# Kernel tuning notes

Hardware: AMD Instinct MI355X
Metric: run time of the kernel (lower is better)

## Reference

```python
import jax, jax.numpy as jnp
import numpy as np
import math

B, T, C = 4, 2048, 2048
HQ, HKV = 16, 4
HD = C // HQ          # 128
REP = HQ // HKV       # 4
EPS = 1e-6


def _rope_tables(seq_len, dim):
    inv_freq = 1.0 / (10000.0 ** (np.arange(0, dim, 2, dtype=np.float32) / dim))
    t = np.arange(seq_len, dtype=np.float32)
    freqs = np.einsum('i,j->ij', t, inv_freq)  # [T, dim/2]
    return jnp.asarray(np.cos(freqs)), jnp.asarray(np.sin(freqs))


def setup_inputs() -> dict:
    key = jax.random.key(0)
    ks = jax.random.split(key, 10)
    s = 0.02
    cos, sin = _rope_tables(T, HD)
    return {
        'x': jax.random.normal(ks[0], (B, T, C), jnp.float32),
        'Wq': jax.random.normal(ks[1], (C, C), jnp.float32) * s,
        'bq': jnp.zeros((C,), jnp.float32),
        'Wk': jax.random.normal(ks[2], (HD * HKV, C), jnp.float32) * s,
        'bk': jnp.zeros((HD * HKV,), jnp.float32),
        'Wv': jax.random.normal(ks[3], (HD * HKV, C), jnp.float32) * s,
        'bv': jnp.zeros((HD * HKV,), jnp.float32),
        'qn_w': jnp.ones((HD,), jnp.float32),
        'kn_w': jnp.ones((HD,), jnp.float32),
        'Wg': jax.random.normal(ks[4], (HD, HD), jnp.float32) * s,
        'bg': jnp.zeros((HD,), jnp.float32),
        'Wo': jax.random.normal(ks[5], (C, C), jnp.float32) * s,
        'bo': jnp.zeros((C,), jnp.float32),
        'cos': cos,
        'sin': sin,
    }


def _apply_rope(x, cos, sin):
    # x: [B,T,H,HD]; cos/sin: [T,HD/2]
    c = cos[None, :, None, :]
    s = sin[None, :, None, :]
    x1, x2 = x[..., ::2], x[..., 1::2]
    return jnp.concatenate([x1 * c - x2 * s, x1 * s + x2 * c], axis=-1)


def _rmsnorm(x, w):
    norm = jnp.mean(x * x, axis=-1, keepdims=True)
    return w * (x * jax.lax.rsqrt(norm + EPS))


def reference(x, Wq, bq, Wk, bk, Wv, bv, qn_w, kn_w, Wg, bg, Wo, bo, cos, sin):
    Bsz, Tlen, _ = x.shape
    q = (x @ Wq.T + bq).reshape(Bsz, Tlen, HQ, HD)
    k = (x @ Wk.T + bk).reshape(Bsz, Tlen, HKV, HD)
    v = (x @ Wv.T + bv).reshape(Bsz, Tlen, HKV, HD)

    q = _rmsnorm(_apply_rope(q, cos, sin), qn_w)
    k = _rmsnorm(_apply_rope(k, cos, sin), kn_w)

    # GQA without materializing repeated K/V: group q heads [B,T,HKV,REP,HD]
    # (repeat_interleave on kv-head dim matches this grouping exactly)
    q5 = q.reshape(Bsz, Tlen, HKV, REP, HD)
    scores = jnp.einsum('btkrd,bskd->bkrts', q5, k) / math.sqrt(HD)

    causal = jnp.tril(jnp.ones((Tlen, Tlen), bool))
    scores = jnp.where(causal, scores, -jnp.inf)
    probs = jax.nn.softmax(scores, axis=-1)

    out = jnp.einsum('bkrts,bskd->btkrd', probs, v).reshape(Bsz, Tlen, HQ, HD)
    gate = jax.nn.sigmoid(out @ Wg.T + bg)
    out = (out * gate).reshape(Bsz, Tlen, C)
    return out @ Wo.T + bo
```

## Files before the change

kernel.cpp:

```cpp
#include <hip/hip_runtime.h>
#include <hip/hip_bf16.h>
#include <math.h>

typedef __attribute__((ext_vector_type(8))) __bf16 bf16x8;
typedef __attribute__((ext_vector_type(4))) float f32x4;

__device__ __forceinline__ void stage16(const void* g, void* l) {
#if __has_builtin(__builtin_amdgcn_global_load_lds)
  __builtin_amdgcn_global_load_lds(
      (const __attribute__((address_space(1))) void*)g,
      (__attribute__((address_space(3))) void*)l, 16, 0, 0);
#else
  *(int4*)l = *(const int4*)g;
#endif
}

__device__ __forceinline__ float sigmoidf_(float x) {
  return 1.0f / (1.0f + __expf(-x));
}

__global__ __launch_bounds__(256) void f2b_kernel(const float* __restrict__ s,
                                                  __bf16* __restrict__ d, int n) {
  int i = (blockIdx.x * blockDim.x + threadIdx.x) * 4;
  if (i >= n) return;
  float4 v = *(const float4*)(s + i);
  union { __bf16 h[4]; int2 p; } u;
  u.h[0] = (__bf16)v.x; u.h[1] = (__bf16)v.y;
  u.h[2] = (__bf16)v.z; u.h[3] = (__bf16)v.w;
  *(int2*)(d + i) = u.p;
}

template <typename OutT>
__global__ __launch_bounds__(512, 1) void gemm256(const __bf16* __restrict__ A,
                                                  const __bf16* __restrict__ Bm,
                                                  const float* __restrict__ bias,
                                                  OutT* __restrict__ C,
                                                  int M, int N, int K, int gx) {
  __shared__ __align__(16) __bf16 Sm[2][2][2][128 * 64];
  const int tid = threadIdx.x, lane = tid & 63, wid = tid >> 6;
  const int wm = wid >> 2, wn = wid & 3;
  const int r = lane & 15, g4 = lane >> 4;
  const int nwg = gridDim.x, qx = nwg >> 3;
  const int wg = (blockIdx.x & 7) * qx + (blockIdx.x >> 3);
  const int m0 = (wg / gx) * 256, n0 = (wg % gx) * 256;

  f32x4 acc[8][4] = {};
  const int NT = K >> 6;

#define STAGE_HALF(buf, which, half, kt)                                          \
  {                                                                               \
    const __bf16* sp_ = (which) ? Bm : A;                                         \
    const int base_ = ((which) ? n0 : m0) + (half) * 128;                         \
    const int k0_ = (kt) << 6;                                                    \
    __bf16* dp_ = &Sm[buf][which][half][0];                                       \
    _Pragma("unroll") for (int i_ = 0; i_ < 2; ++i_) {                            \
      int c_ = i_ * 512 + tid;                                                    \
      int row_ = c_ >> 3, slot_ = c_ & 7;                                         \
      stage16(sp_ + (size_t)(base_ + row_) * K + k0_ + ((slot_ ^ (row_ & 7)) << 3), \
              dp_ + c_ * 8);                                                      \
    }                                                                             \
  }
#define LDSW(base, row, kk) \
  (*(const bf16x8*)&(base)[(row) * 64 + ((((kk) * 4 + g4) ^ ((row) & 7)) << 3)])

  STAGE_HALF(0, 0, 0, 0) STAGE_HALF(0, 0, 1, 0) STAGE_HALF(0, 1, 0, 0) STAGE_HALF(0, 1, 1, 0)

  const int brow = (wn & 1) * 64;
  bf16x8 af[4][2], bfr[2][2];

  for (int kt = 0; kt < NT; ++kt) {
    const int cur = kt & 1, nxt = cur ^ 1;
    const bool more = (kt + 1) < NT;
    const __bf16* Ah = &Sm[cur][0][wm][0];
    const __bf16* Bh = &Sm[cur][1][wn >> 1][0];

    if (more) STAGE_HALF(nxt, 0, 0, kt + 1)
    if (more) { asm volatile("s_waitcnt vmcnt(2)" ::: "memory"); }
    else      { asm volatile("s_waitcnt vmcnt(0)" ::: "memory"); }
    __builtin_amdgcn_s_barrier();
    asm volatile("" ::: "memory");
#pragma unroll
    for (int m = 0; m < 4; ++m)
#pragma unroll
      for (int kk = 0; kk < 2; ++kk) af[m][kk] = LDSW(Ah, m * 16 + r, kk);
#pragma unroll
    for (int n = 0; n < 2; ++n)
#pragma unroll
      for (int kk = 0; kk < 2; ++kk) bfr[n][kk] = LDSW(Bh, brow + n * 16 + r, kk);
    asm volatile("s_waitcnt lgkmcnt(0)" ::: "memory");
    __builtin_amdgcn_sched_barrier(0);
    __builtin_amdgcn_s_setprio(1);
#pragma unroll
    for (int m = 0; m < 4; ++m)
#pragma unroll
      for (int n = 0; n < 2; ++n)
#pragma unroll
        for (int kk = 0; kk < 2; ++kk)
          acc[m][n] = __builtin_amdgcn_mfma_f32_16x16x32_bf16(af[m][kk], bfr[n][kk],
                                                              acc[m][n], 0, 0, 0);
    __builtin_amdgcn_s_setprio(0);
    __builtin_amdgcn_s_barrier();

#pragma unroll
    for (int n = 0; n < 2; ++n)
#pragma unroll
      for (int kk = 0; kk < 2; ++kk) bfr[n][kk] = LDSW(Bh, brow + (2 + n) * 16 + r, kk);
    if (more) STAGE_HALF(nxt, 0, 1, kt + 1)
    asm volatile("s_waitcnt lgkmcnt(0)" ::: "memory");
    __builtin_amdgcn_sched_barrier(0);
    __builtin_amdgcn_s_setprio(1);
#pragma unroll
    for (int m = 0; m < 4; ++m)
#pragma unroll
      for (int n = 0; n < 2; ++n)
#pragma unroll
        for (int kk = 0; kk < 2; ++kk)
          acc[m][2 + n] = __builtin_amdgcn_mfma_f32_16x16x32_bf16(af[m][kk], bfr[n][kk],
                                                                  acc[m][2 + n], 0, 0, 0);
    __builtin_amdgcn_s_setprio(0);
    __builtin_amdgcn_s_barrier();

#pragma unroll
    for (int m = 0; m < 4; ++m)
#pragma unroll
      for (int kk = 0; kk < 2; ++kk) af[m][kk] = LDSW(Ah, (4 + m) * 16 + r, kk);
#pragma unroll
    for (int n = 0; n < 2; ++n)
#pragma unroll
      for (int kk = 0; kk < 2; ++kk) bfr[n][kk] = LDSW(Bh, brow + n * 16 + r, kk);
    if (more) STAGE_HALF(nxt, 1, 0, kt + 1)
    asm volatile("s_waitcnt lgkmcnt(0)" ::: "memory");
    __builtin_amdgcn_sched_barrier(0);
    __builtin_amdgcn_s_setprio(1);
#pragma unroll
    for (int m = 0; m < 4; ++m)
#pragma unroll
      for (int n = 0; n < 2; ++n)
#pragma unroll
        for (int kk = 0; kk < 2; ++kk)
          acc[4 + m][n] = __builtin_amdgcn_mfma_f32_16x16x32_bf16(af[m][kk], bfr[n][kk],
                                                                  acc[4 + m][n], 0, 0, 0);
    __builtin_amdgcn_s_setprio(0);
    __builtin_amdgcn_s_barrier();

#pragma unroll
    for (int n = 0; n < 2; ++n)
#pragma unroll
      for (int kk = 0; kk < 2; ++kk) bfr[n][kk] = LDSW(Bh, brow + (2 + n) * 16 + r, kk);
    if (more) STAGE_HALF(nxt, 1, 1, kt + 1)
    asm volatile("s_waitcnt lgkmcnt(0)" ::: "memory");
    __builtin_amdgcn_sched_barrier(0);
    __builtin_amdgcn_s_setprio(1);
#pragma unroll
    for (int m = 0; m < 4; ++m)
#pragma unroll
      for (int n = 0; n < 2; ++n)
#pragma unroll
        for (int kk = 0; kk < 2; ++kk)
          acc[4 + m][2 + n] = __builtin_amdgcn_mfma_f32_16x16x32_bf16(af[m][kk], bfr[n][kk],
                                                                      acc[4 + m][2 + n], 0, 0, 0);
    __builtin_amdgcn_s_setprio(0);
    __builtin_amdgcn_s_barrier();
  }

  const int rq = lane >> 4;
#pragma unroll
  for (int m = 0; m < 8; ++m)
#pragma unroll
    for (int n = 0; n < 4; ++n) {
      int col = n0 + wn * 64 + n * 16 + r;
      float bv = bias ? bias[col] : 0.0f;
#pragma unroll
      for (int j = 0; j < 4; ++j) {
        int row = m0 + wm * 128 + m * 16 + rq * 4 + j;
        C[(size_t)row * N + col] = (OutT)(acc[m][n][j] + bv);
      }
    }
#undef STAGE_HALF
#undef LDSW
}

__global__ __launch_bounds__(256) void vtrans(const __bf16* __restrict__ Y,
                                              __bf16* __restrict__ VT) {
  __shared__ __bf16 tile[32][66];
  const int t0 = blockIdx.x * 64;
  const int d0 = blockIdx.y * 32;
  const int bh = blockIdx.z;
  const int b = bh >> 2, hv = bh & 3;
  const __bf16* src = Y + (size_t)b * 2048 * 3072 + 2560 + hv * 128 + d0;
  const int dd = threadIdx.x & 31, tt = threadIdx.x >> 5;
#pragma unroll
  for (int p = 0; p < 8; ++p) {
    int t = tt + p * 8;
    tile[dd][t] = src[(size_t)(t0 + t) * 3072 + dd];
  }
  __syncthreads();
  __bf16* dst = VT + ((size_t)bh * 128 + d0) * 2048 + t0;
  const int oc = threadIdx.x & 63, orr = threadIdx.x >> 6;
#pragma unroll
  for (int p = 0; p < 8; ++p) {
    int d = orr + p * 4;
    dst[(size_t)d * 2048 + oc] = tile[d][oc];
  }
}

__global__ __launch_bounds__(256) void rope_norm(const __bf16* __restrict__ Y,
                                                 const float* __restrict__ cosT,
                                                 const float* __restrict__ sinT,
                                                 const float* __restrict__ qn,
                                                 const float* __restrict__ kn,
                                                 __bf16* __restrict__ qat,
                                                 __bf16* __restrict__ kat) {
  const int tok = blockIdx.x;
  const int b = tok >> 11, t = tok & 2047;
  const int wv = threadIdx.x >> 6, l = threadIdx.x & 63;
  const __bf16* row = Y + (size_t)tok * 3072;
  const float c = cosT[t * 64 + l], s = sinT[t * 64 + l];
#pragma unroll
  for (int i = 0; i < 5; ++i) {
    const int h = wv + i * 4;
    const bool isq = h < 16;
    const int base = isq ? h * 128 : 2048 + (h - 16) * 128;
    union { uint32_t u; __bf16 h2[2]; } p;
    p.u = *(const uint32_t*)(row + base + 2 * l);
    float x1 = (float)p.h2[0], x2 = (float)p.h2[1];
    float v1 = x1 * c - x2 * s;
    float v2 = x1 * s + x2 * c;
    float ss = v1 * v1 + v2 * v2;
#pragma unroll
    for (int o = 32; o >= 1; o >>= 1) ss += __shfl_xor(ss, o, 64);
    float rms = rsqrtf(ss * (1.0f / 128.0f) + 1e-6f);
    float w1 = isq ? qn[l] : kn[l];
    float w2 = isq ? qn[64 + l] : kn[64 + l];
    size_t ob = isq ? (((size_t)b * 16 + h) * 2048 + t) * 128
                    : (((size_t)b * 4 + (h - 16)) * 2048 + t) * 128;
    __bf16* dst = isq ? qat : kat;
    dst[ob + l] = (__bf16)(w1 * v1 * rms);
    dst[ob + 64 + l] = (__bf16)(w2 * v2 * rms);
  }
}

__global__ __launch_bounds__(512, 4) void attn5(const __bf16* __restrict__ Q,
                                                const __bf16* __restrict__ Kg,
                                                const __bf16* __restrict__ VTg,
                                                __bf16* __restrict__ ab) {
  __shared__ __align__(16) __bf16 Kt[2][64 * 128];
  __shared__ __align__(16) __bf16 Vt[2][128 * 64];
  __shared__ __align__(16) __bf16 Ps[8 * 16 * 64];
  const int tid = threadIdx.x, lane = tid & 63, wv = tid >> 6;
  const int L = blockIdx.x;
  const int xcd = L & 7, slot = L >> 3;
  const int group = xcd * 2 + (slot >> 5);
  const int idx = slot & 31;
  const int b = group >> 2, hkv = group & 3;
  const int hq = hkv * 4 + (idx >> 3);
  const int p = idx & 7;
  const __bf16* qp = Q + ((size_t)b * 16 + hq) * 2048 * 128;
  const __bf16* kp = Kg + ((size_t)b * 4 + hkv) * 2048 * 128;
  const __bf16* vp = VTg + ((size_t)b * 4 + hkv) * 128 * 2048;
  const int r = lane & 15, g4 = lane >> 4, ks = g4 * 8;
  const float SCALE = 0.08838834764831845f;

#define STAGE_TILE(bi, kv0)                                                  \
  {                                                                          \
    __bf16* Kb = &Kt[bi][0];                                                 \
    __bf16* Vb = &Vt[bi][0];                                                 \
    _Pragma("unroll") for (int i = 0; i < 2; ++i) {                          \
      int c = i * 512 + tid;                                                 \
      int row = c >> 4, slot_ = c & 15;                                      \
      int gco = ((slot_ ^ (row & 7)) << 3);                                  \
      stage16(kp + (size_t)((kv0) + row) * 128 + gco, &Kb[c * 8]);           \
    }                                                                        \
    _Pragma("unroll") for (int i = 0; i < 2; ++i) {                          \
      int c = i * 512 + tid;                                                 \
      int row = c >> 3, slot_ = c & 7;                                       \
      int gco = ((slot_ ^ (row & 7)) << 3);                                  \
      stage16(vp + (size_t)row * 2048 + (kv0) + gco, &Vb[c * 8]);            \
    }                                                                        \
  }

  for (int half = 0; half < 2; ++half) {
    const int qt = half == 0 ? (15 - p) : p;
    const int q0 = qt * 128 + wv * 16;

    bf16x8 qf[4];
#pragma unroll
    for (int kk = 0; kk < 4; ++kk)
      qf[kk] = *(const bf16x8*)(qp + (size_t)(q0 + r) * 128 + kk * 32 + ks);

    f32x4 Of[8] = {};
    float mrow[4] = {-1e30f, -1e30f, -1e30f, -1e30f};
    float lrow[4] = {0.f, 0.f, 0.f, 0.f};

    const int nt = 2 * qt + 2;
    STAGE_TILE(0, 0);
    int cur = 0;
    for (int t = 0; t < nt; ++t) {
      const int kv0 = t * 64;
      if (t + 1 < nt) {
        STAGE_TILE(cur ^ 1, (t + 1) * 64);
        asm volatile("s_waitcnt vmcnt(4)" ::: "memory");
      } else {
        asm volatile("s_waitcnt vmcnt(0)" ::: "memory");
      }
      __builtin_amdgcn_s_barrier();

      const __bf16* Kb = &Kt[cur][0];
      const __bf16* Vb = &Vt[cur][0];

      f32x4 s[4];
      __builtin_amdgcn_s_setprio(1);
#pragma unroll
      for (int kj = 0; kj < 4; ++kj) {
        f32x4 sa = {};
        int krow = kj * 16 + r;
#pragma unroll
        for (int kk = 0; kk < 4; ++kk) {
          int slot_ = (kk * 4 + g4) ^ (r & 7);
          bf16x8 kf = *(const bf16x8*)&Kb[krow * 128 + slot_ * 8];
          sa = __builtin_amdgcn_mfma_f32_16x16x32_bf16(qf[kk], kf, sa, 0, 0, 0);
        }
        s[kj] = sa;
      }
      __builtin_amdgcn_s_setprio(0);
#pragma unroll
      for (int kj = 0; kj < 4; ++kj)
#pragma unroll
        for (int j = 0; j < 4; ++j) s[kj][j] *= SCALE;
      if (kv0 + 63 > q0) {
#pragma unroll
        for (int kj = 0; kj < 4; ++kj)
#pragma unroll
          for (int j = 0; j < 4; ++j) {
            int kv = kv0 + kj * 16 + r;
            int qrow = q0 + g4 * 4 + j;
            if (kv > qrow) s[kj][j] = -1e30f;
          }
      }
      float tm[4], rs[4];
#pragma unroll
      for (int j = 0; j < 4; ++j)
        tm[j] = fmaxf(fmaxf(s[0][j], s[1][j]), fmaxf(s[2][j], s[3][j]));
#pragma unroll
      for (int o = 8; o >= 1; o >>= 1)
#pragma unroll
        for (int j = 0; j < 4; ++j) tm[j] = fmaxf(tm[j], __shfl_xor(tm[j], o, 64));
      float growth = fmaxf(fmaxf(tm[0] - mrow[0], tm[1] - mrow[1]),
                           fmaxf(tm[2] - mrow[2], tm[3] - mrow[3]));
      if (__any(growth > 8.0f)) {
#pragma unroll
        for (int j = 0; j < 4; ++j) {
          float mn = fmaxf(mrow[j], tm[j]);
          float corr = __expf(mrow[j] - mn);
          mrow[j] = mn;
          lrow[j] *= corr;
#pragma unroll
          for (int f = 0; f < 8; ++f) Of[f][j] *= corr;
        }
      }
#pragma unroll
      for (int j = 0; j < 4; ++j) {
        float acc = 0.f;
#pragma unroll
        for (int kj = 0; kj < 4; ++kj) { s[kj][j] = __expf(s[kj][j] - mrow[j]); acc += s[kj][j]; }
        rs[j] = acc;
      }
#pragma unroll
      for (int o = 8; o >= 1; o >>= 1)
#pragma unroll
        for (int j = 0; j < 4; ++j) rs[j] += __shfl_xor(rs[j], o, 64);
#pragma unroll
      for (int j = 0; j < 4; ++j) lrow[j] += rs[j];

      __bf16* pw = &Ps[wv * 16 * 64];
#pragma unroll
      for (int kj = 0; kj < 4; ++kj)
#pragma unroll
        for (int j = 0; j < 4; ++j) {
          int qr = g4 * 4 + j;
          int kvl = kj * 16 + r;
          int sl = (kvl >> 3) ^ (qr & 7);
          pw[qr * 64 + sl * 8 + (kvl & 7)] = (__bf16)s[kj][j];
        }
      __builtin_amdgcn_s_setprio(1);
#pragma unroll
      for (int kvj = 0; kvj < 2; ++kvj) {
        int sl = (kvj * 4 + g4) ^ (r & 7);
        bf16x8 pa = *(const bf16x8*)&pw[r * 64 + sl * 8];
#pragma unroll
        for (int dn = 0; dn < 8; ++dn) {
          bf16x8 vb = *(const bf16x8*)&Vb[(dn * 16 + r) * 64 + sl * 8];
          Of[dn] = __builtin_amdgcn_mfma_f32_16x16x32_bf16(pa, vb, Of[dn], 0, 0, 0);
        }
      }
      __builtin_amdgcn_s_setprio(0);
      __builtin_amdgcn_s_barrier();
      cur ^= 1;
    }

    float inv[4];
#pragma unroll
    for (int j = 0; j < 4; ++j) inv[j] = 1.0f / lrow[j];
#pragma unroll
    for (int dn = 0; dn < 8; ++dn)
#pragma unroll
      for (int j = 0; j < 4; ++j) {
        int row = q0 + g4 * 4 + j;
        int d = dn * 16 + r;
        ab[(((size_t)b * 2048 + row) * 16 + hq) * 128 + d] = (__bf16)(Of[dn][j] * inv[j]);
      }
  }
#undef STAGE_TILE
}

__global__ __launch_bounds__(256) void gate_fused(const __bf16* __restrict__ a,
                                                  const __bf16* __restrict__ WgB,
                                                  const float* __restrict__ bg,
                                                  __bf16* __restrict__ og) {
  __shared__ __align__(16) __bf16 Wl[128 * 128];
  const int tid = threadIdx.x, lane = tid & 63, wv = tid >> 6;
  const int r = lane & 15, g4 = lane >> 4, ks = g4 * 8;
#pragma unroll
  for (int i = 0; i < 8; ++i) {
    int c = i * 256 + tid;
    int row = c >> 4, slot = c & 15;
    *(bf16x8*)&Wl[row * 128 + ((slot ^ (row & 7)) << 3)] =
        *(const bf16x8*)&WgB[row * 128 + slot * 8];
  }
  __syncthreads();
  const size_t r0 = (size_t)blockIdx.x * 64 + wv * 16;
  bf16x8 af[4];
#pragma unroll
  for (int kk = 0; kk < 4; ++kk)
    af[kk] = *(const bf16x8*)(a + (r0 + r) * 128 + kk * 32 + ks);
  f32x4 acc[8] = {};
#pragma unroll
  for (int dn = 0; dn < 8; ++dn) {
    int row = dn * 16 + r;
#pragma unroll
    for (int kk = 0; kk < 4; ++kk) {
      bf16x8 bf_ = *(const bf16x8*)&Wl[row * 128 + (((kk * 4 + g4) ^ (row & 7)) << 3)];
      acc[dn] = __builtin_amdgcn_mfma_f32_16x16x32_bf16(af[kk], bf_, acc[dn], 0, 0, 0);
    }
  }
#pragma unroll
  for (int dn = 0; dn < 8; ++dn) {
    float bgv = bg[dn * 16 + r];
#pragma unroll
    for (int j = 0; j < 4; ++j) {
      size_t row = r0 + g4 * 4 + j;
      int col = dn * 16 + r;
      float gv = sigmoidf_(acc[dn][j] + bgv);
      float av = (float)a[row * 128 + col];
      og[row * 128 + col] = (__bf16)(av * gv);
    }
  }
}

extern "C" void kernel_launch(void* const* d_in, const int* in_sizes, int n_in,
                              void* d_out, int out_size, void* d_ws, size_t ws_size,
                              hipStream_t stream) {
  const float* x    = (const float*)d_in[0];
  const float* Wq   = (const float*)d_in[1];
  const float* bq   = (const float*)d_in[2];
  const float* Wk   = (const float*)d_in[3];
  const float* bk   = (const float*)d_in[4];
  const float* Wv   = (const float*)d_in[5];
  const float* bv   = (const float*)d_in[6];
  const float* qn   = (const float*)d_in[7];
  const float* kn   = (const float*)d_in[8];
  const float* Wg   = (const float*)d_in[9];
  const float* bg   = (const float*)d_in[10];
  const float* Wo   = (const float*)d_in[11];
  const float* bo   = (const float*)d_in[12];
  const float* cosT = (const float*)d_in[13];
  const float* sinT = (const float*)d_in[14];

  char* ws = (char*)d_ws;
  constexpr size_t OFF_WQKV = 0;
  constexpr size_t OFF_WO   = OFF_WQKV + 3072ull * 2048 * 2;
  constexpr size_t OFF_WG   = OFF_WO + 2048ull * 2048 * 2;
  constexpr size_t OFF_BQKV = OFF_WG + 128ull * 128 * 2;
  constexpr size_t OFF_XB   = OFF_BQKV + 16384;
  constexpr size_t OFF_Y    = OFF_XB + 8192ull * 2048 * 2;
  constexpr size_t OFF_QAT  = OFF_Y + 8192ull * 3072 * 2;
  constexpr size_t OFF_KAT  = OFF_QAT + 4ull * 16 * 2048 * 128 * 2;
  constexpr size_t OFF_VT   = OFF_KAT + 4ull * 4 * 2048 * 128 * 2;
  constexpr size_t OFF_AB   = OFF_VT + 4ull * 4 * 2048 * 128 * 2;

  __bf16* WQKVb = (__bf16*)(ws + OFF_WQKV);
  __bf16* WOb   = (__bf16*)(ws + OFF_WO);
  __bf16* WGb   = (__bf16*)(ws + OFF_WG);
  float*  BQKV  = (float*)(ws + OFF_BQKV);
  __bf16* XB    = (__bf16*)(ws + OFF_XB);
  __bf16* Y     = (__bf16*)(ws + OFF_Y);
  __bf16* QAT   = (__bf16*)(ws + OFF_QAT);
  __bf16* KAT   = (__bf16*)(ws + OFF_KAT);
  __bf16* VT    = (__bf16*)(ws + OFF_VT);
  __bf16* ABuf  = (__bf16*)(ws + OFF_AB);
  __bf16* OGB   = (__bf16*)(ws + OFF_XB);

  f2b_kernel<<<16384, 256, 0, stream>>>(x, XB, 16777216);
  f2b_kernel<<<4096, 256, 0, stream>>>(Wq, WQKVb, 4194304);
  f2b_kernel<<<1024, 256, 0, stream>>>(Wk, WQKVb + 2048ull * 2048, 1048576);
  f2b_kernel<<<1024, 256, 0, stream>>>(Wv, WQKVb + 2560ull * 2048, 1048576);
  f2b_kernel<<<4096, 256, 0, stream>>>(Wo, WOb, 4194304);
  f2b_kernel<<<16, 256, 0, stream>>>(Wg, WGb, 16384);
  hipMemcpyAsync(BQKV, bq, 2048 * 4, hipMemcpyDeviceToDevice, stream);
  hipMemcpyAsync(BQKV + 2048, bk, 512 * 4, hipMemcpyDeviceToDevice, stream);
  hipMemcpyAsync(BQKV + 2560, bv, 512 * 4, hipMemcpyDeviceToDevice, stream);

  gemm256<__bf16><<<384, 512, 0, stream>>>(XB, WQKVb, BQKV, Y, 8192, 3072, 2048, 12);

  rope_norm<<<8192, 256, 0, stream>>>(Y, cosT, sinT, qn, kn, QAT, KAT);
  vtrans<<<dim3(32, 4, 16), 256, 0, stream>>>(Y, VT);

  attn5<<<512, 512, 0, stream>>>(QAT, KAT, VT, ABuf);

  gate_fused<<<2048, 256, 0, stream>>>(ABuf, WGb, bg, OGB);

  gemm256<float><<<256, 512, 0, stream>>>(OGB, WOb, bo, (float*)d_out, 8192, 2048, 2048, 8);
}
```

Baseline: 438.4 us.

## Merge prep launches, add 128-row QKV GEMM, fuse rope/vtrans, fold softmax scale

Replaces six conversion launches and three memcpys with a single prep kernel, and merges rope_norm and vtrans into one launch. The QKV projection now uses a new 128x256-tile GEMM with 768 workgroups instead of 384 larger tiles, for better CU fill. The softmax scale and log2(e) are folded into Q during rope, so attention uses exp2f and drops a per-score multiply. These are several unrelated changes, and the scale folding adds a little rounding because the pre-scaled Q is stored in bf16.

```diff
diff --git a/kernel.cpp b/kernel.cpp
--- a/kernel.cpp
+++ b/kernel.cpp
@@ -19,15 +19,50 @@
   return 1.0f / (1.0f + __expf(-x));
 }
 
-__global__ __launch_bounds__(256) void f2b_kernel(const float* __restrict__ s,
-                                                  __bf16* __restrict__ d, int n) {
-  int i = (blockIdx.x * blockDim.x + threadIdx.x) * 4;
-  if (i >= n) return;
-  float4 v = *(const float4*)(s + i);
+__device__ __forceinline__ void f2b4(const float* __restrict__ s, __bf16* __restrict__ d) {
+  float4 v = *(const float4*)s;
   union { __bf16 h[4]; int2 p; } u;
   u.h[0] = (__bf16)v.x; u.h[1] = (__bf16)v.y;
   u.h[2] = (__bf16)v.z; u.h[3] = (__bf16)v.w;
-  *(int2*)(d + i) = u.p;
+  *(int2*)d = u.p;
+}
+
+__global__ __launch_bounds__(256) void prep(const float* __restrict__ x,
+                                            const float* __restrict__ Wq,
+                                            const float* __restrict__ Wk,
+                                            const float* __restrict__ Wv,
+                                            const float* __restrict__ Wo,
+                                            const float* __restrict__ Wg,
+                                            const float* __restrict__ bq,
+                                            const float* __restrict__ bk,
+                                            const float* __restrict__ bv,
+                                            __bf16* __restrict__ XB,
+                                            __bf16* __restrict__ WQKVb,
+                                            __bf16* __restrict__ WOb,
+                                            __bf16* __restrict__ WGb,
+                                            float* __restrict__ BQKV) {
+  int c = blockIdx.x * 256 + threadIdx.x;
+  if (c >= 6820608) return;
+  if (c < 4194304) {
+    f2b4(x + (size_t)c * 4, XB + (size_t)c * 4);
+  } else if (c < 5242880) {
+    int e = (c - 4194304) * 4;  f2b4(Wq + e, WQKVb + e);
+  } else if (c < 5505024) {
+    int e = (c - 5242880) * 4;  f2b4(Wk + e, WQKVb + 4194304 + e);
+  } else if (c < 5767168) {
+    int e = (c - 5505024) * 4;  f2b4(Wv + e, WQKVb + 5242880 + e);
+  } else if (c < 6815744) {
+    int e = (c - 5767168) * 4;  f2b4(Wo + e, WOb + e);
+  } else if (c < 6819840) {
+    int e = (c - 6815744) * 4;  f2b4(Wg + e, WGb + e);
+  } else {
+    int e = (c - 6819840) * 4;
+    float4 v;
+    if (e < 2048)      v = *(const float4*)(bq + e);
+    else if (e < 2560) v = *(const float4*)(bk + (e - 2048));
+    else               v = *(const float4*)(bv + (e - 2560));
+    *(float4*)(BQKV + e) = v;
+  }
 }
 
 template <typename OutT>
@@ -180,67 +215,176 @@
 #undef LDSW
 }
 
-__global__ __launch_bounds__(256) void vtrans(const __bf16* __restrict__ Y,
-                                              __bf16* __restrict__ VT) {
+__global__ __launch_bounds__(512, 1) void gemm128(const __bf16* __restrict__ A,
+                                                  const __bf16* __restrict__ Bm,
+                                                  const float* __restrict__ bias,
+                                                  __bf16* __restrict__ C,
+                                                  int M, int N, int K, int gx) {
+  __shared__ __align__(16) __bf16 Sm[2][3][128 * 64];
+  const int tid = threadIdx.x, lane = tid & 63, wid = tid >> 6;
+  const int wm = wid >> 2, wn = wid & 3;
+  const int r = lane & 15, g4 = lane >> 4;
+  const int nwg = gridDim.x, qx = nwg >> 3;
+  const int wg = (blockIdx.x & 7) * qx + (blockIdx.x >> 3);
+  const int m0 = (wg / gx) * 128, n0 = (wg % gx) * 256;
+
+  f32x4 acc[4][4] = {};
+  const int NT = K >> 6;
+
+#define STAGE_SEG(buf, seg, sp, rowbase, kt)                                        \
+  {                                                                                 \
+    __bf16* dp_ = &Sm[buf][seg][0];                                                 \
+    const int k0_ = (kt) << 6;                                                      \
+    _Pragma("unroll") for (int i_ = 0; i_ < 2; ++i_) {                              \
+      int c_ = i_ * 512 + tid;                                                      \
+      int row_ = c_ >> 3, slot_ = c_ & 7;                                           \
+      stage16((sp) + (size_t)((rowbase) + row_) * K + k0_ + ((slot_ ^ (row_ & 7)) << 3), \
+              dp_ + c_ * 8);                                                        \
+    }                                                                               \
+  }
+#define LDSW(base, row, kk) \
+  (*(const bf16x8*)&(base)[(row) * 64 + ((((kk) * 4 + g4) ^ ((row) & 7)) << 3)])
+
+  STAGE_SEG(0, 0, A, m0, 0) STAGE_SEG(0, 1, Bm, n0, 0) STAGE_SEG(0, 2, Bm, n0 + 128, 0)
+
+  const int bseg = 1 + (wn >> 1);
+  const int brow = (wn & 1) * 64;
+  bf16x8 af[4][2], bfr[2][2];
+
+  for (int kt = 0; kt < NT; ++kt) {
+    const int cur = kt & 1, nxt = cur ^ 1;
+    const bool more = (kt + 1) < NT;
+    const __bf16* Ah = &Sm[cur][0][0];
+    const __bf16* Bh = &Sm[cur][bseg][0];
+
+    if (more) { STAGE_SEG(nxt, 0, A, m0, kt + 1) STAGE_SEG(nxt, 1, Bm, n0, kt + 1) }
+    if (more) { asm volatile("s_waitcnt vmcnt(4)" ::: "memory"); }
+    else      { asm volatile("s_waitcnt vmcnt(0)" ::: "memory"); }
+    __builtin_amdgcn_s_barrier();
+    asm volatile("" ::: "memory");
+#pragma unroll
+    for (int m = 0; m < 4; ++m)
+#pragma unroll
+      for (int kk = 0; kk < 2; ++kk) af[m][kk] = LDSW(Ah, wm * 64 + m * 16 + r, kk);
+#pragma unroll
+    for (int n = 0; n < 2; ++n)
+#pragma unroll
+      for (int kk = 0; kk < 2; ++kk) bfr[n][kk] = LDSW(Bh, brow + n * 16 + r, kk);
+    asm volatile("s_waitcnt lgkmcnt(0)" ::: "memory");
+    __builtin_amdgcn_sched_barrier(0);
+    __builtin_amdgcn_s_setprio(1);
+#pragma unroll
+    for (int m = 0; m < 4; ++m)
+#pragma unroll
+      for (int n = 0; n < 2; ++n)
+#pragma unroll
+        for (int kk = 0; kk < 2; ++kk)
+          acc[m][n] = __builtin_amdgcn_mfma_f32_16x16x32_bf16(af[m][kk], bfr[n][kk],
+                                                              acc[m][n], 0, 0, 0);
+    __builtin_amdgcn_s_setprio(0);
+    __builtin_amdgcn_s_barrier();
+
+#pragma unroll
+    for (int n = 0; n < 2; ++n)
+#pragma unroll
+      for (int kk = 0; kk < 2; ++kk) bfr[n][kk] = LDSW(Bh, brow + (2 + n) * 16 + r, kk);
+    if (more) STAGE_SEG(nxt, 2, Bm, n0 + 128, kt + 1)
+    asm volatile("s_waitcnt lgkmcnt(0)" ::: "memory");
+    __builtin_amdgcn_sched_barrier(0);
+    __builtin_amdgcn_s_setprio(1);
+#pragma unroll
+    for (int m = 0; m < 4; ++m)
+#pragma unroll
+      for (int n = 0; n < 2; ++n)
+#pragma unroll
+        for (int kk = 0; kk < 2; ++kk)
+          acc[m][2 + n] = __builtin_amdgcn_mfma_f32_16x16x32_bf16(af[m][kk], bfr[n][kk],
+                                                                  acc[m][2 + n], 0, 0, 0);
+    __builtin_amdgcn_s_setprio(0);
+    __builtin_amdgcn_s_barrier();
+  }
+
+  const int rq = lane >> 4;
+#pragma unroll
+  for (int m = 0; m < 4; ++m)
+#pragma unroll
+    for (int n = 0; n < 4; ++n) {
+      int col = n0 + wn * 64 + n * 16 + r;
+      float bv = bias ? bias[col] : 0.0f;
+#pragma unroll
+      for (int j = 0; j < 4; ++j) {
+        int row = m0 + wm * 64 + m * 16 + rq * 4 + j;
+        C[(size_t)row * N + col] = (__bf16)(acc[m][n][j] + bv);
+      }
+    }
+#undef STAGE_SEG
+#undef LDSW
+}
+
+__global__ __launch_bounds__(256) void rope_vt(const __bf16* __restrict__ Y,
+                                               const float* __restrict__ cosT,
+                                               const float* __restrict__ sinT,
+                                               const float* __restrict__ qn,
+                                               const float* __restrict__ kn,
+                                               __bf16* __restrict__ qat,
+                                               __bf16* __restrict__ kat,
+                                               __bf16* __restrict__ VT) {
   __shared__ __bf16 tile[32][66];
-  const int t0 = blockIdx.x * 64;
-  const int d0 = blockIdx.y * 32;
-  const int bh = blockIdx.z;
-  const int b = bh >> 2, hv = bh & 3;
-  const __bf16* src = Y + (size_t)b * 2048 * 3072 + 2560 + hv * 128 + d0;
-  const int dd = threadIdx.x & 31, tt = threadIdx.x >> 5;
-#pragma unroll
-  for (int p = 0; p < 8; ++p) {
-    int t = tt + p * 8;
-    tile[dd][t] = src[(size_t)(t0 + t) * 3072 + dd];
-  }
-  __syncthreads();
-  __bf16* dst = VT + ((size_t)bh * 128 + d0) * 2048 + t0;
-  const int oc = threadIdx.x & 63, orr = threadIdx.x >> 6;
-#pragma unroll
-  for (int p = 0; p < 8; ++p) {
-    int d = orr + p * 4;
-    dst[(size_t)d * 2048 + oc] = tile[d][oc];
-  }
-}
-
-__global__ __launch_bounds__(256) void rope_norm(const __bf16* __restrict__ Y,
-                                                 const float* __restrict__ cosT,
-                                                 const float* __restrict__ sinT,
-                                                 const float* __restrict__ qn,
-                                                 const float* __restrict__ kn,
-                                                 __bf16* __restrict__ qat,
-                                                 __bf16* __restrict__ kat) {
-  const int tok = blockIdx.x;
-  const int b = tok >> 11, t = tok & 2047;
-  const int wv = threadIdx.x >> 6, l = threadIdx.x & 63;
-  const __bf16* row = Y + (size_t)tok * 3072;
-  const float c = cosT[t * 64 + l], s = sinT[t * 64 + l];
-#pragma unroll
-  for (int i = 0; i < 5; ++i) {
-    const int h = wv + i * 4;
-    const bool isq = h < 16;
-    const int base = isq ? h * 128 : 2048 + (h - 16) * 128;
-    union { uint32_t u; __bf16 h2[2]; } p;
-    p.u = *(const uint32_t*)(row + base + 2 * l);
-    float x1 = (float)p.h2[0], x2 = (float)p.h2[1];
-    float v1 = x1 * c - x2 * s;
-    float v2 = x1 * s + x2 * c;
-    float ss = v1 * v1 + v2 * v2;
-#pragma unroll
-    for (int o = 32; o >= 1; o >>= 1) ss += __shfl_xor(ss, o, 64);
-    float rms = rsqrtf(ss * (1.0f / 128.0f) + 1e-6f);
-    float w1 = isq ? qn[l] : kn[l];
-    float w2 = isq ? qn[64 + l] : kn[64 + l];
-    size_t ob = isq ? (((size_t)b * 16 + h) * 2048 + t) * 128
-                    : (((size_t)b * 4 + (h - 16)) * 2048 + t) * 128;
-    __bf16* dst = isq ? qat : kat;
-    dst[ob + l] = (__bf16)(w1 * v1 * rms);
-    dst[ob + 64 + l] = (__bf16)(w2 * v2 * rms);
-  }
-}
-
-__global__ __launch_bounds__(512, 4) void attn5(const __bf16* __restrict__ Q,
+  if (blockIdx.x < 8192) {
+    const int tok = blockIdx.x;
+    const int b = tok >> 11, t = tok & 2047;
+    const int wv = threadIdx.x >> 6, l = threadIdx.x & 63;
+    const __bf16* row = Y + (size_t)tok * 3072;
+    const float c = cosT[t * 64 + l], s = sinT[t * 64 + l];
+    const float QS = 0.08838834764831845f * 1.4426950408889634f;
+#pragma unroll
+    for (int i = 0; i < 5; ++i) {
+      const int h = wv + i * 4;
+      const bool isq = h < 16;
+      const int base = isq ? h * 128 : 2048 + (h - 16) * 128;
+      union { uint32_t u; __bf16 h2[2]; } p;
+      p.u = *(const uint32_t*)(row + base + 2 * l);
+      float x1 = (float)p.h2[0], x2 = (float)p.h2[1];
+      float v1 = x1 * c - x2 * s;
+      float v2 = x1 * s + x2 * c;
+      float ss = v1 * v1 + v2 * v2;
+#pragma unroll
+      for (int o = 32; o >= 1; o >>= 1) ss += __shfl_xor(ss, o, 64);
+      float rms = rsqrtf(ss * (1.0f / 128.0f) + 1e-6f);
+      if (isq) rms *= QS;
+      float w1 = isq ? qn[l] : kn[l];
+      float w2 = isq ? qn[64 + l] : kn[64 + l];
+      size_t ob = isq ? (((size_t)b * 16 + h) * 2048 + t) * 128
+                      : (((size_t)b * 4 + (h - 16)) * 2048 + t) * 128;
+      __bf16* dst = isq ? qat : kat;
+      dst[ob + l] = (__bf16)(w1 * v1 * rms);
+      dst[ob + 64 + l] = (__bf16)(w2 * v2 * rms);
+    }
+  } else {
+    const int i = blockIdx.x - 8192;
+    const int t0 = (i & 31) * 64;
+    const int d0 = ((i >> 5) & 3) * 32;
+    const int bh = i >> 7;
+    const int b = bh >> 2, hv = bh & 3;
+    const __bf16* src = Y + (size_t)b * 2048 * 3072 + 2560 + hv * 128 + d0;
+    const int dd = threadIdx.x & 31, tt = threadIdx.x >> 5;
+#pragma unroll
+    for (int p = 0; p < 8; ++p) {
+      int t = tt + p * 8;
+      tile[dd][t] = src[(size_t)(t0 + t) * 3072 + dd];
+    }
+    __syncthreads();
+    __bf16* dst = VT + ((size_t)bh * 128 + d0) * 2048 + t0;
+    const int oc = threadIdx.x & 63, orr = threadIdx.x >> 6;
+#pragma unroll
+    for (int p = 0; p < 8; ++p) {
+      int d = orr + p * 4;
+      dst[(size_t)d * 2048 + oc] = tile[d][oc];
+    }
+  }
+}
+
+__global__ __launch_bounds__(512, 4) void attn6(const __bf16* __restrict__ Q,
                                                 const __bf16* __restrict__ Kg,
                                                 const __bf16* __restrict__ VTg,
                                                 __bf16* __restrict__ ab) {
@@ -259,7 +403,6 @@
   const __bf16* kp = Kg + ((size_t)b * 4 + hkv) * 2048 * 128;
   const __bf16* vp = VTg + ((size_t)b * 4 + hkv) * 128 * 2048;
   const int r = lane & 15, g4 = lane >> 4, ks = g4 * 8;
-  const float SCALE = 0.08838834764831845f;
 
 #define STAGE_TILE(bi, kv0)                                                  \
   {                                                                          \
@@ -323,10 +466,6 @@
         s[kj] = sa;
       }
       __builtin_amdgcn_s_setprio(0);
-#pragma unroll
-      for (int kj = 0; kj < 4; ++kj)
-#pragma unroll
-        for (int j = 0; j < 4; ++j) s[kj][j] *= SCALE;
       if (kv0 + 63 > q0) {
 #pragma unroll
         for (int kj = 0; kj < 4; ++kj)
@@ -351,7 +490,7 @@
 #pragma unroll
         for (int j = 0; j < 4; ++j) {
           float mn = fmaxf(mrow[j], tm[j]);
-          float corr = __expf(mrow[j] - mn);
+          float corr = exp2f(mrow[j] - mn);
           mrow[j] = mn;
           lrow[j] *= corr;
 #pragma unroll
@@ -362,7 +501,7 @@
       for (int j = 0; j < 4; ++j) {
         float acc = 0.f;
 #pragma unroll
-        for (int kj = 0; kj < 4; ++kj) { s[kj][j] = __expf(s[kj][j] - mrow[j]); acc += s[kj][j]; }
+        for (int kj = 0; kj < 4; ++kj) { s[kj][j] = exp2f(s[kj][j] - mrow[j]); acc += s[kj][j]; }
         rs[j] = acc;
       }
 #pragma unroll
@@ -500,22 +639,14 @@
   __bf16* ABuf  = (__bf16*)(ws + OFF_AB);
   __bf16* OGB   = (__bf16*)(ws + OFF_XB);
 
-  f2b_kernel<<<16384, 256, 0, stream>>>(x, XB, 16777216);
-  f2b_kernel<<<4096, 256, 0, stream>>>(Wq, WQKVb, 4194304);
-  f2b_kernel<<<1024, 256, 0, stream>>>(Wk, WQKVb + 2048ull * 2048, 1048576);
-  f2b_kernel<<<1024, 256, 0, stream>>>(Wv, WQKVb + 2560ull * 2048, 1048576);
-  f2b_kernel<<<4096, 256, 0, stream>>>(Wo, WOb, 4194304);
-  f2b_kernel<<<16, 256, 0, stream>>>(Wg, WGb, 16384);
-  hipMemcpyAsync(BQKV, bq, 2048 * 4, hipMemcpyDeviceToDevice, stream);
-  hipMemcpyAsync(BQKV + 2048, bk, 512 * 4, hipMemcpyDeviceToDevice, stream);
-  hipMemcpyAsync(BQKV + 2560, bv, 512 * 4, hipMemcpyDeviceToDevice, stream);
-
-  gemm256<__bf16><<<384, 512, 0, stream>>>(XB, WQKVb, BQKV, Y, 8192, 3072, 2048, 12);
-
-  rope_norm<<<8192, 256, 0, stream>>>(Y, cosT, sinT, qn, kn, QAT, KAT);
-  vtrans<<<dim3(32, 4, 16), 256, 0, stream>>>(Y, VT);
-
-  attn5<<<512, 512, 0, stream>>>(QAT, KAT, VT, ABuf);
+  prep<<<26643, 256, 0, stream>>>(x, Wq, Wk, Wv, Wo, Wg, bq, bk, bv,
+                                  XB, WQKVb, WOb, WGb, BQKV);
+
+  gemm128<<<768, 512, 0, stream>>>(XB, WQKVb, BQKV, Y, 8192, 3072, 2048, 12);
+
+  rope_vt<<<10240, 256, 0, stream>>>(Y, cosT, sinT, qn, kn, QAT, KAT, VT);
+
+  attn6<<<512, 512, 0, stream>>>(QAT, KAT, VT, ABuf);
 
   gate_fused<<<2048, 256, 0, stream>>>(ABuf, WGb, bg, OGB);
 
```

Measured after the change: 430.0 us. About the same (-1.9%).
